# Optimization experiments

Hardware: AMD Instinct MI355X
Metric: run time of the kernel (lower is better)

Reference implementation:

```python
import jax, jax.numpy as jnp
import numpy as np

N = 1048576
FEA = 128
N0 = 16384


def setup_inputs() -> dict:
    key = jax.random.key(0)
    k1, k2 = jax.random.split(key)
    atom_fea = jax.random.normal(k1, (N, FEA), dtype=jnp.float32)
    segment_ids = jnp.sort(jax.random.randint(k2, (N,), 0, N0, dtype=jnp.int32))
    return {"atom_fea": atom_fea, "segment_ids": segment_ids, "num_crystals": N0}


def reference(atom_fea, segment_ids, num_crystals):
    # Fused segment-mean: equivalent to [mean(atom_fea[idx]) for idx in crystal_atom_idx]
    sums = jax.ops.segment_sum(atom_fea, segment_ids, num_segments=num_crystals)  # (N0, FEA)
    counts = jax.ops.segment_sum(jnp.ones((atom_fea.shape[0],), atom_fea.dtype),
                                 segment_ids, num_segments=num_crystals)  # (N0,)
    counts = jnp.maximum(counts, 1.0)  # guard empty segments (original assumes none)
    return sums / counts[:, None]
```

## Files before the change

kernel.cpp:

```cpp
#include <hip/hip_runtime.h>

#define FEA 128

__global__ __launch_bounds__(256) void segmean_kernel(
    const float* __restrict__ atom_fea,
    const int*   __restrict__ ids,
    float*       __restrict__ out,
    int n_atoms, int n_seg)
{
    const int wave = threadIdx.x >> 6;
    const int lane = threadIdx.x & 63;
    const int seg  = blockIdx.x * 4 + wave;
    if (seg >= n_seg) return;

    int lo0 = 0, hi0 = n_atoms;
    int lo1 = 0, hi1 = n_atoms;
    while ((lo0 < hi0) | (lo1 < hi1)) {
        if (lo0 < hi0) {
            int mid = (lo0 + hi0) >> 1;
            if (ids[mid] < seg) lo0 = mid + 1; else hi0 = mid;
        }
        if (lo1 < hi1) {
            int mid = (lo1 + hi1) >> 1;
            if (ids[mid] < seg + 1) lo1 = mid + 1; else hi1 = mid;
        }
    }
    const int start = lo0;
    const int n     = lo1 - lo0;

    const int a_sub = lane >> 5;
    const int g     = lane & 31;

    const float4* base = (const float4*)atom_fea + (size_t)start * 32 + g;

    float4 acc0 = make_float4(0.f, 0.f, 0.f, 0.f);
    float4 acc1 = make_float4(0.f, 0.f, 0.f, 0.f);

    int k = a_sub;
    for (; k + 2 < n; k += 4) {
        float4 v0 = base[(size_t)k       * 32];
        float4 v1 = base[(size_t)(k + 2) * 32];
        acc0.x += v0.x; acc0.y += v0.y; acc0.z += v0.z; acc0.w += v0.w;
        acc1.x += v1.x; acc1.y += v1.y; acc1.z += v1.z; acc1.w += v1.w;
    }
    for (; k < n; k += 2) {
        float4 v = base[(size_t)k * 32];
        acc0.x += v.x; acc0.y += v.y; acc0.z += v.z; acc0.w += v.w;
    }

    acc0.x += acc1.x; acc0.y += acc1.y; acc0.z += acc1.z; acc0.w += acc1.w;

    acc0.x += __shfl_xor(acc0.x, 32, 64);
    acc0.y += __shfl_xor(acc0.y, 32, 64);
    acc0.z += __shfl_xor(acc0.z, 32, 64);
    acc0.w += __shfl_xor(acc0.w, 32, 64);

    const float invn = 1.0f / (float)((n > 0) ? n : 1);

    if (a_sub == 0) {
        float4 r;
        r.x = acc0.x * invn; r.y = acc0.y * invn;
        r.z = acc0.z * invn; r.w = acc0.w * invn;
        ((float4*)out)[(size_t)seg * 32 + g] = r;
    }
}

extern "C" void kernel_launch(void* const* d_in, const int* in_sizes, int n_in,
                              void* d_out, int out_size, void* d_ws, size_t ws_size,
                              hipStream_t stream) {
    const float* atom_fea = (const float*)d_in[0];
    const int*   ids      = (const int*)d_in[1];
    float*       out      = (float*)d_out;

    const int n_atoms = in_sizes[1];
    const int n_seg   = out_size / FEA;

    const int blocks = (n_seg + 3) / 4;
    segmean_kernel<<<blocks, 256, 0, stream>>>(atom_fea, ids, out, n_atoms, n_seg);
}
```

Before: 124.1 us.

## Precompute segment boundaries in a pre-pass instead of per-wave binary search

Adds a pre-kernel that scans the sorted segment ids and writes each segment's start offset into a workspace array. The main kernel then reads two offsets instead of running two 20-step dependent binary searches over global memory. The accumulation loop is also unrolled to four independent float4 loads per lane to raise memory-level parallelism. This costs an extra kernel launch and a pass over the ids. It falls back to the binary-search kernel when the workspace is too small.

```diff
diff --git a/kernel.cpp b/kernel.cpp
--- a/kernel.cpp
+++ b/kernel.cpp
@@ -2,7 +2,99 @@
 
 #define FEA 128
 
+__global__ __launch_bounds__(256) void build_bounds_kernel(
+    const int* __restrict__ ids, int* __restrict__ B, int n_atoms, int n_seg)
+{
+    const int t  = blockIdx.x * blockDim.x + threadIdx.x;
+    const int i0 = t * 4;
+    if (i0 >= n_atoms) return;
+
+    int prev = (i0 == 0) ? -1 : ids[i0 - 1];
+
+    if (i0 + 3 < n_atoms) {
+        const int4 v = *(const int4*)(ids + i0);
+        const int cur[4] = {v.x, v.y, v.z, v.w};
+        #pragma unroll
+        for (int j = 0; j < 4; ++j) {
+            if (cur[j] != prev)
+                for (int s = prev + 1; s <= cur[j]; ++s) B[s] = i0 + j;
+            prev = cur[j];
+        }
+        if (i0 + 4 == n_atoms)
+            for (int s = prev + 1; s <= n_seg; ++s) B[s] = n_atoms;
+    } else {
+        for (int j = 0; j < 4 && i0 + j < n_atoms; ++j) {
+            const int c = ids[i0 + j];
+            if (c != prev)
+                for (int s = prev + 1; s <= c; ++s) B[s] = i0 + j;
+            prev = c;
+        }
+        if (i0 + 4 >= n_atoms)
+            for (int s = prev + 1; s <= n_seg; ++s) B[s] = n_atoms;
+    }
+}
+
 __global__ __launch_bounds__(256) void segmean_kernel(
+    const float* __restrict__ atom_fea,
+    const int*   __restrict__ B,
+    float*       __restrict__ out,
+    int n_seg)
+{
+    const int wave = threadIdx.x >> 6;
+    const int lane = threadIdx.x & 63;
+    const int seg  = blockIdx.x * 4 + wave;
+    if (seg >= n_seg) return;
+
+    const int start = B[seg];
+    const int n     = B[seg + 1] - start;
+
+    const int a_sub = lane >> 5;
+    const int g     = lane & 31;
+
+    const float4* base = (const float4*)atom_fea + (size_t)start * 32 + g;
+
+    float4 a0 = make_float4(0.f, 0.f, 0.f, 0.f);
+    float4 a1 = make_float4(0.f, 0.f, 0.f, 0.f);
+    float4 a2 = make_float4(0.f, 0.f, 0.f, 0.f);
+    float4 a3 = make_float4(0.f, 0.f, 0.f, 0.f);
+
+    int k = a_sub;
+    for (; k + 6 < n; k += 8) {
+        float4 v0 = base[(size_t)k       * 32];
+        float4 v1 = base[(size_t)(k + 2) * 32];
+        float4 v2 = base[(size_t)(k + 4) * 32];
+        float4 v3 = base[(size_t)(k + 6) * 32];
+        a0.x += v0.x; a0.y += v0.y; a0.z += v0.z; a0.w += v0.w;
+        a1.x += v1.x; a1.y += v1.y; a1.z += v1.z; a1.w += v1.w;
+        a2.x += v2.x; a2.y += v2.y; a2.z += v2.z; a2.w += v2.w;
+        a3.x += v3.x; a3.y += v3.y; a3.z += v3.z; a3.w += v3.w;
+    }
+    for (; k < n; k += 2) {
+        float4 v = base[(size_t)k * 32];
+        a0.x += v.x; a0.y += v.y; a0.z += v.z; a0.w += v.w;
+    }
+
+    a0.x += a1.x + a2.x + a3.x;
+    a0.y += a1.y + a2.y + a3.y;
+    a0.z += a1.z + a2.z + a3.z;
+    a0.w += a1.w + a2.w + a3.w;
+
+    a0.x += __shfl_xor(a0.x, 32, 64);
+    a0.y += __shfl_xor(a0.y, 32, 64);
+    a0.z += __shfl_xor(a0.z, 32, 64);
+    a0.w += __shfl_xor(a0.w, 32, 64);
+
+    const float invn = 1.0f / (float)((n > 0) ? n : 1);
+
+    if (a_sub == 0) {
+        float4 r;
+        r.x = a0.x * invn; r.y = a0.y * invn;
+        r.z = a0.z * invn; r.w = a0.w * invn;
+        ((float4*)out)[(size_t)seg * 32 + g] = r;
+    }
+}
+
+__global__ __launch_bounds__(256) void segmean_bsearch_kernel(
     const float* __restrict__ atom_fea,
     const int*   __restrict__ ids,
     float*       __restrict__ out,
@@ -13,54 +105,33 @@
     const int seg  = blockIdx.x * 4 + wave;
     if (seg >= n_seg) return;
 
-    int lo0 = 0, hi0 = n_atoms;
-    int lo1 = 0, hi1 = n_atoms;
+    int lo0 = 0, hi0 = n_atoms, lo1 = 0, hi1 = n_atoms;
     while ((lo0 < hi0) | (lo1 < hi1)) {
-        if (lo0 < hi0) {
-            int mid = (lo0 + hi0) >> 1;
-            if (ids[mid] < seg) lo0 = mid + 1; else hi0 = mid;
-        }
-        if (lo1 < hi1) {
-            int mid = (lo1 + hi1) >> 1;
-            if (ids[mid] < seg + 1) lo1 = mid + 1; else hi1 = mid;
-        }
+        if (lo0 < hi0) { int m = (lo0 + hi0) >> 1; if (ids[m] < seg)     lo0 = m + 1; else hi0 = m; }
+        if (lo1 < hi1) { int m = (lo1 + hi1) >> 1; if (ids[m] < seg + 1) lo1 = m + 1; else hi1 = m; }
     }
     const int start = lo0;
     const int n     = lo1 - lo0;
 
     const int a_sub = lane >> 5;
     const int g     = lane & 31;
-
     const float4* base = (const float4*)atom_fea + (size_t)start * 32 + g;
 
-    float4 acc0 = make_float4(0.f, 0.f, 0.f, 0.f);
-    float4 acc1 = make_float4(0.f, 0.f, 0.f, 0.f);
-
-    int k = a_sub;
-    for (; k + 2 < n; k += 4) {
-        float4 v0 = base[(size_t)k       * 32];
-        float4 v1 = base[(size_t)(k + 2) * 32];
-        acc0.x += v0.x; acc0.y += v0.y; acc0.z += v0.z; acc0.w += v0.w;
-        acc1.x += v1.x; acc1.y += v1.y; acc1.z += v1.z; acc1.w += v1.w;
+    float4 a0 = make_float4(0.f, 0.f, 0.f, 0.f);
+    for (int k = a_sub; k < n; k += 2) {
+        float4 v = base[(size_t)k * 32];
+        a0.x += v.x; a0.y += v.y; a0.z += v.z; a0.w += v.w;
     }
-    for (; k < n; k += 2) {
-        float4 v = base[(size_t)k * 32];
-        acc0.x += v.x; acc0.y += v.y; acc0.z += v.z; acc0.w += v.w;
-    }
-
-    acc0.x += acc1.x; acc0.y += acc1.y; acc0.z += acc1.z; acc0.w += acc1.w;
-
-    acc0.x += __shfl_xor(acc0.x, 32, 64);
-    acc0.y += __shfl_xor(acc0.y, 32, 64);
-    acc0.z += __shfl_xor(acc0.z, 32, 64);
-    acc0.w += __shfl_xor(acc0.w, 32, 64);
+    a0.x += __shfl_xor(a0.x, 32, 64);
+    a0.y += __shfl_xor(a0.y, 32, 64);
+    a0.z += __shfl_xor(a0.z, 32, 64);
+    a0.w += __shfl_xor(a0.w, 32, 64);
 
     const float invn = 1.0f / (float)((n > 0) ? n : 1);
-
     if (a_sub == 0) {
         float4 r;
-        r.x = acc0.x * invn; r.y = acc0.y * invn;
-        r.z = acc0.z * invn; r.w = acc0.w * invn;
+        r.x = a0.x * invn; r.y = a0.y * invn;
+        r.z = a0.z * invn; r.w = a0.w * invn;
         ((float4*)out)[(size_t)seg * 32 + g] = r;
     }
 }
@@ -75,6 +146,16 @@
     const int n_atoms = in_sizes[1];
     const int n_seg   = out_size / FEA;
 
-    const int blocks = (n_seg + 3) / 4;
-    segmean_kernel<<<blocks, 256, 0, stream>>>(atom_fea, ids, out, n_atoms, n_seg);
+    const size_t bounds_bytes = (size_t)(n_seg + 1) * sizeof(int);
+    const int    seg_blocks   = (n_seg + 3) / 4;
+
+    if (ws_size >= bounds_bytes) {
+        int* B = (int*)d_ws;
+        const int n_thr    = (n_atoms + 3) / 4;
+        const int b_blocks = (n_thr + 255) / 256;
+        build_bounds_kernel<<<b_blocks, 256, 0, stream>>>(ids, B, n_atoms, n_seg);
+        segmean_kernel<<<seg_blocks, 256, 0, stream>>>(atom_fea, B, out, n_seg);
+    } else {
+        segmean_bsearch_kernel<<<seg_blocks, 256, 0, stream>>>(atom_fea, ids, out, n_atoms, n_seg);
+    }
 }
```

Result: faster. 109.8 us (-11.5%).

## Split segment mean into boundary prologue and fixed-size atom-chunk kernel

Applied to the files above, without the earlier changes.

Adds a prologue kernel that computes segment start offsets in workspace and zeros the output rows of empty segments and of segments that span chunk boundaries. The main kernel then gives each wave a fixed chunk of 128 atoms, writing directly for segments fully inside the chunk and using atomicAdd for segments that cross chunk edges. This replaces the per-segment binary search and balances work when segment sizes vary, and it adds nontemporal loads with more accumulators. The cost is an extra kernel launch, float atomics that make results order-dependent, and reliance on workspace being available.

```diff
diff --git a/kernel.cpp b/kernel.cpp
--- a/kernel.cpp
+++ b/kernel.cpp
@@ -1,8 +1,129 @@
 #include <hip/hip_runtime.h>
 
-#define FEA 128
+#define FEA   128
+#define CHUNK 128
 
-__global__ __launch_bounds__(256) void segmean_kernel(
+typedef float f4 __attribute__((ext_vector_type(4)));
+
+__global__ __launch_bounds__(256) void prologue_kernel(
+    const int* __restrict__ ids, int* __restrict__ B, float* __restrict__ out,
+    int n_atoms, int n_seg, int b_blocks, int n_chunks)
+{
+    if ((int)blockIdx.x < b_blocks) {
+        const int t  = blockIdx.x * 256 + threadIdx.x;
+        const int i0 = t * 4;
+        if (i0 >= n_atoms) return;
+        int prev = (i0 == 0) ? -1 : ids[i0 - 1];
+        #pragma unroll
+        for (int j = 0; j < 4; ++j) {
+            const int i = i0 + j;
+            if (i >= n_atoms) break;
+            const int cur = ids[i];
+            if (cur != prev) {
+                for (int s = prev + 1; s <= cur; ++s) B[s] = i;
+                for (int s = prev + 1; s < cur; ++s) {
+                    f4* row = (f4*)(out + (size_t)s * FEA);
+                    const f4 z = {0.f, 0.f, 0.f, 0.f};
+                    for (int q = 0; q < FEA / 4; ++q) row[q] = z;
+                }
+                prev = cur;
+            }
+        }
+        if (i0 + 4 >= n_atoms) {
+            for (int s = prev + 1; s <= n_seg; ++s) B[s] = n_atoms;
+            for (int s = prev + 1; s < n_seg; ++s) {
+                f4* row = (f4*)(out + (size_t)s * FEA);
+                const f4 z = {0.f, 0.f, 0.f, 0.f};
+                for (int q = 0; q < FEA / 4; ++q) row[q] = z;
+            }
+        }
+    } else {
+        const int t = ((int)blockIdx.x - b_blocks) * 256 + threadIdx.x;
+        const int b = t >> 5;
+        const int g = t & 31;
+        const int p = (b + 1) * CHUNK;
+        if (b >= n_chunks - 1 || p >= n_atoms) return;
+        const int sl = ids[p - 1];
+        const int sr = ids[p];
+        if (sl == sr) {
+            const f4 z = {0.f, 0.f, 0.f, 0.f};
+            ((f4*)(out + (size_t)sr * FEA))[g] = z;
+        }
+    }
+}
+
+__global__ __launch_bounds__(256) void segmean_chunk_kernel(
+    const float* __restrict__ atom_fea,
+    const int*   __restrict__ ids,
+    const int*   __restrict__ B,
+    float*       __restrict__ out,
+    int n_atoms)
+{
+    const int wid   = (blockIdx.x * 256 + threadIdx.x) >> 6;
+    const int lane  = threadIdx.x & 63;
+    const int c0    = wid * CHUNK;
+    if (c0 >= n_atoms) return;
+    const int c1    = min(c0 + CHUNK, n_atoms);
+    const int a_sub = lane >> 5;
+    const int g     = lane & 31;
+
+    int s   = ids[c0];
+    int pos = c0;
+
+    while (pos < c1) {
+        const int segS = B[s];
+        const int segE = B[s + 1];
+        const int e    = min(segE, c1);
+        const int m    = e - pos;
+
+        const f4* base = (const f4*)atom_fea + (size_t)pos * (FEA / 4) + g;
+
+        f4 a0 = {0.f, 0.f, 0.f, 0.f};
+        f4 a1 = {0.f, 0.f, 0.f, 0.f};
+        f4 a2 = {0.f, 0.f, 0.f, 0.f};
+        f4 a3 = {0.f, 0.f, 0.f, 0.f};
+
+        int k = a_sub;
+        for (; k + 6 < m; k += 8) {
+            f4 v0 = __builtin_nontemporal_load(base + (size_t)k       * 32);
+            f4 v1 = __builtin_nontemporal_load(base + (size_t)(k + 2) * 32);
+            f4 v2 = __builtin_nontemporal_load(base + (size_t)(k + 4) * 32);
+            f4 v3 = __builtin_nontemporal_load(base + (size_t)(k + 6) * 32);
+            a0 += v0; a1 += v1; a2 += v2; a3 += v3;
+        }
+        for (; k < m; k += 2)
+            a0 += __builtin_nontemporal_load(base + (size_t)k * 32);
+
+        a0 += a1 + a2 + a3;
+
+        a0[0] += __shfl_xor(a0[0], 32, 64);
+        a0[1] += __shfl_xor(a0[1], 32, 64);
+        a0[2] += __shfl_xor(a0[2], 32, 64);
+        a0[3] += __shfl_xor(a0[3], 32, 64);
+
+        const int   n_total = segE - segS;
+        const float invn    = 1.0f / (float)((n_total > 0) ? n_total : 1);
+
+        if (segS >= c0 && segE <= c1) {
+            if (a_sub == 0) {
+                f4 r = a0 * invn;
+                ((f4*)(out + (size_t)s * FEA))[g] = r;
+            }
+        } else {
+            if (a_sub == 0) {
+                float* dst = out + (size_t)s * FEA + g * 4;
+                atomicAdd(dst + 0, a0[0] * invn);
+                atomicAdd(dst + 1, a0[1] * invn);
+                atomicAdd(dst + 2, a0[2] * invn);
+                atomicAdd(dst + 3, a0[3] * invn);
+            }
+        }
+        pos = e;
+        ++s;
+    }
+}
+
+__global__ __launch_bounds__(256) void segmean_bsearch_kernel(
     const float* __restrict__ atom_fea,
     const int*   __restrict__ ids,
     float*       __restrict__ out,
@@ -13,55 +134,31 @@
     const int seg  = blockIdx.x * 4 + wave;
     if (seg >= n_seg) return;
 
-    int lo0 = 0, hi0 = n_atoms;
-    int lo1 = 0, hi1 = n_atoms;
+    int lo0 = 0, hi0 = n_atoms, lo1 = 0, hi1 = n_atoms;
     while ((lo0 < hi0) | (lo1 < hi1)) {
-        if (lo0 < hi0) {
-            int mid = (lo0 + hi0) >> 1;
-            if (ids[mid] < seg) lo0 = mid + 1; else hi0 = mid;
-        }
-        if (lo1 < hi1) {
-            int mid = (lo1 + hi1) >> 1;
-            if (ids[mid] < seg + 1) lo1 = mid + 1; else hi1 = mid;
-        }
+        if (lo0 < hi0) { int m = (lo0 + hi0) >> 1; if (ids[m] < seg)     lo0 = m + 1; else hi0 = m; }
+        if (lo1 < hi1) { int m = (lo1 + hi1) >> 1; if (ids[m] < seg + 1) lo1 = m + 1; else hi1 = m; }
     }
     const int start = lo0;
     const int n     = lo1 - lo0;
 
     const int a_sub = lane >> 5;
     const int g     = lane & 31;
+    const f4* base  = (const f4*)atom_fea + (size_t)start * (FEA / 4) + g;
 
-    const float4* base = (const float4*)atom_fea + (size_t)start * 32 + g;
+    f4 a0 = {0.f, 0.f, 0.f, 0.f};
+    for (int k = a_sub; k < n; k += 2)
+        a0 += *(base + (size_t)k * 32);
 
-    float4 acc0 = make_float4(0.f, 0.f, 0.f, 0.f);
-    float4 acc1 = make_float4(0.f, 0.f, 0.f, 0.f);
-
-    int k = a_sub;
-    for (; k + 2 < n; k += 4) {
-        float4 v0 = base[(size_t)k       * 32];
-        float4 v1 = base[(size_t)(k + 2) * 32];
-        acc0.x += v0.x; acc0.y += v0.y; acc0.z += v0.z; acc0.w += v0.w;
-        acc1.x += v1.x; acc1.y += v1.y; acc1.z += v1.z; acc1.w += v1.w;
-    }
-    for (; k < n; k += 2) {
-        float4 v = base[(size_t)k * 32];
-        acc0.x += v.x; acc0.y += v.y; acc0.z += v.z; acc0.w += v.w;
-    }
-
-    acc0.x += acc1.x; acc0.y += acc1.y; acc0.z += acc1.z; acc0.w += acc1.w;
-
-    acc0.x += __shfl_xor(acc0.x, 32, 64);
-    acc0.y += __shfl_xor(acc0.y, 32, 64);
-    acc0.z += __shfl_xor(acc0.z, 32, 64);
-    acc0.w += __shfl_xor(acc0.w, 32, 64);
+    a0[0] += __shfl_xor(a0[0], 32, 64);
+    a0[1] += __shfl_xor(a0[1], 32, 64);
+    a0[2] += __shfl_xor(a0[2], 32, 64);
+    a0[3] += __shfl_xor(a0[3], 32, 64);
 
     const float invn = 1.0f / (float)((n > 0) ? n : 1);
-
     if (a_sub == 0) {
-        float4 r;
-        r.x = acc0.x * invn; r.y = acc0.y * invn;
-        r.z = acc0.z * invn; r.w = acc0.w * invn;
-        ((float4*)out)[(size_t)seg * 32 + g] = r;
+        f4 r = a0 * invn;
+        ((f4*)(out + (size_t)seg * FEA))[g] = r;
     }
 }
 
@@ -75,6 +172,25 @@
     const int n_atoms = in_sizes[1];
     const int n_seg   = out_size / FEA;
 
-    const int blocks = (n_seg + 3) / 4;
-    segmean_kernel<<<blocks, 256, 0, stream>>>(atom_fea, ids, out, n_atoms, n_seg);
+    const size_t bounds_bytes = (size_t)(n_seg + 1) * sizeof(int);
+
+    if (ws_size >= bounds_bytes) {
+        int* B = (int*)d_ws;
+
+        const int n_chunks = (n_atoms + CHUNK - 1) / CHUNK;
+        const int b_blocks = (((n_atoms + 3) / 4) + 255) / 256;
+        const int z_thr    = (n_chunks > 1) ? (n_chunks - 1) * 32 : 0;
+        const int z_blocks = (z_thr + 255) / 256;
+
+        prologue_kernel<<<b_blocks + z_blocks, 256, 0, stream>>>(
+            ids, B, out, n_atoms, n_seg, b_blocks, n_chunks);
+
+        const int m_blocks = (n_chunks + 3) / 4;
+        segmean_chunk_kernel<<<m_blocks, 256, 0, stream>>>(
+            atom_fea, ids, B, out, n_atoms);
+    } else {
+        const int seg_blocks = (n_seg + 3) / 4;
+        segmean_bsearch_kernel<<<seg_blocks, 256, 0, stream>>>(
+            atom_fea, ids, out, n_atoms, n_seg);
+    }
 }
```

Result: faster. 109.3 us (-11.9%).
